# Kernel tuning notes

Hardware: AMD Instinct MI355X
Metric: run time of the kernel (lower is better)

## Reference

```python
import jax, jax.numpy as jnp
import numpy as np

E, D, H, B = 8, 64, 512, 32768  # n_experts, state_dim, hidden width, batch
IN = D + 3  # x, t, sin(omega*t), cos(omega*t)


def setup_inputs() -> dict:
    key = jax.random.key(0)
    ks = jax.random.split(key, 12)
    s = 0.02
    return {
        "t": jax.random.uniform(ks[0], (1,), dtype=jnp.float32),
        "x": jax.random.normal(ks[1], (B, D), dtype=jnp.float32),
        "expert_weights": jax.random.uniform(ks[2], (B, E), dtype=jnp.float32),
        "omega": jnp.arange(1, E + 1, dtype=jnp.float32),  # omega_i = i+1
        "W1": jax.random.normal(ks[3], (E, H, IN), dtype=jnp.float32) * s,
        "b1": jnp.zeros((E, H), dtype=jnp.float32),
        "W2": jax.random.normal(ks[4], (E, H, H), dtype=jnp.float32) * s,
        "b2": jnp.zeros((E, H), dtype=jnp.float32),
        "W3": jax.random.normal(ks[5], (E, H, H), dtype=jnp.float32) * s,
        "b3": jnp.zeros((E, H), dtype=jnp.float32),
        "W4": jax.random.normal(ks[6], (E, D, H), dtype=jnp.float32) * s,
        "b4": jnp.zeros((E, D), dtype=jnp.float32),
    }


def reference(t, x, expert_weights, omega, W1, b1, W2, b2, W3, b3, W4, b4):
    # Dense path of ExpertODEEnsemble.forward: all experts active.
    nB = x.shape[0]
    tb = jnp.broadcast_to(t, (nB,))                       # (B,)
    wt = omega[:, None] * tb[None, :]                     # (E, B)
    # Per-expert inputs: [x, t, sin(wt), cos(wt)] -> (E, B, D+3)
    xe = jnp.broadcast_to(x[None], (E, nB, D))
    te = jnp.broadcast_to(tb[None, :, None], (E, nB, 1))
    inp = jnp.concatenate([xe, te, jnp.sin(wt)[..., None], jnp.cos(wt)[..., None]], axis=-1)
    h = jnp.tanh(jnp.einsum('ebi,ehi->ebh', inp, W1) + b1[:, None, :])
    h = jnp.tanh(jnp.einsum('ebh,egh->ebg', h, W2) + b2[:, None, :])
    h = jnp.tanh(jnp.einsum('ebh,egh->ebg', h, W3) + b3[:, None, :])
    dyn = jnp.einsum('ebh,edh->ebd', h, W4) + b4[:, None, :]   # (E, B, D)
    # Weighted combine: sum_e w[b,e] * dyn[e,b,:]
    dx_dt = jnp.einsum('be,ebd->bd', expert_weights, dyn)
    return dx_dt
```

## Files before the change

### kernel.cpp

```cpp
#include <hip/hip_runtime.h>
#include <hip/hip_bf16.h>


typedef unsigned short ushort_t;
typedef unsigned int u32;
typedef unsigned long long u64;
typedef __attribute__((ext_vector_type(8))) short short8;
typedef __attribute__((ext_vector_type(4))) float floatx4;
typedef __attribute__((ext_vector_type(16))) float floatx16;
typedef __attribute__((ext_vector_type(4))) int intx4;

#define W1A_OFF 0u
#define W2A_OFF 524288u
#define W3A_OFF 4718592u
#define W4A_OFF 8912896u
#define XB_OFF  9437184u
#define B1E_OFF 13631488u

static __device__ __forceinline__ u32 pk2bf(float a, float b) {
  union { __hip_bfloat162 h; u32 u; } v;
  v.h = __float22bfloat162_rn(make_float2(a, b));
  return v.u;
}

static __device__ __forceinline__ float pade_tanh(float x) {
  float x2 = x * x;
  float num = __builtin_fmaf(x2, __builtin_fmaf(x2, 1.0f, 105.0f), 945.0f);
  float den = __builtin_fmaf(x2, __builtin_fmaf(x2, 15.0f, 420.0f), 945.0f);
  return x * num * __builtin_amdgcn_rcpf(den);
}

static __device__ __forceinline__ void ald16(const void* g, void* l) {
  __builtin_amdgcn_global_load_lds((__attribute__((address_space(1))) void*)g,
                                   (__attribute__((address_space(3))) void*)l,
                                   16, 0, 0);
}

static __device__ __forceinline__ floatx16 mfma32(short8 a, short8 b, floatx16 c) {
  return __builtin_amdgcn_mfma_f32_32x32x16_bf16(a, b, c, 0, 0, 0);
}

__global__ __launch_bounds__(256) void prep_kernel(
    const float* __restrict__ t, const float* __restrict__ x,
    const float* __restrict__ omega, const float* __restrict__ W1,
    const float* __restrict__ b1, const float* __restrict__ W2,
    const float* __restrict__ W3, const float* __restrict__ W4,
    char* __restrict__ ws) {
  int i = blockIdx.x * 256 + threadIdx.x;
  if (i < 32768) {
    int e = i >> 12, rem = i & 4095, outr = rem >> 3, kg = rem & 7;
    int lane = (outr & 31) | ((kg & 1) << 5);
    int w = outr >> 7, ol = (outr >> 5) & 3, kc = kg >> 1;
    int dest = e * 4096 + ((w * 4 + kc) * 4 + ol) * 64 + lane;
    const float* s = W1 + (e * 512 + outr) * 67 + kg * 8;
    ((intx4*)(ws + W1A_OFF))[dest] = (intx4){
        (int)pk2bf(s[0], s[1]), (int)pk2bf(s[2], s[3]),
        (int)pk2bf(s[4], s[5]), (int)pk2bf(s[6], s[7])};
    return;
  }
  i -= 32768;
  if (i < 262144) {
    int e = i >> 15, rem = i & 32767, outr = rem >> 6, kg = rem & 63;
    int lane = (outr & 31) | ((kg & 1) << 5);
    int w = outr >> 7, ol = (outr >> 5) & 3, kc = kg >> 1;
    int dest = e * 32768 + ((w * 32 + kc) * 4 + ol) * 64 + lane;
    const floatx4* s = (const floatx4*)(W2 + ((e << 9) + outr) * 512 + (kg << 3));
    floatx4 lo = s[0], hi = s[1];
    ((intx4*)(ws + W2A_OFF))[dest] = (intx4){
        (int)pk2bf(lo[0], lo[1]), (int)pk2bf(lo[2], lo[3]),
        (int)pk2bf(hi[0], hi[1]), (int)pk2bf(hi[2], hi[3])};
    return;
  }
  i -= 262144;
  if (i < 262144) {
    int e = i >> 15, rem = i & 32767, outr = rem >> 6, kg = rem & 63;
    int lane = (outr & 31) | ((kg & 1) << 5);
    int w = outr >> 7, ol = (outr >> 5) & 3, kc = kg >> 1;
    int dest = e * 32768 + ((w * 32 + kc) * 4 + ol) * 64 + lane;
    const floatx4* s = (const floatx4*)(W3 + ((e << 9) + outr) * 512 + (kg << 3));
    floatx4 lo = s[0], hi = s[1];
    ((intx4*)(ws + W3A_OFF))[dest] = (intx4){
        (int)pk2bf(lo[0], lo[1]), (int)pk2bf(lo[2], lo[3]),
        (int)pk2bf(hi[0], hi[1]), (int)pk2bf(hi[2], hi[3])};
    return;
  }
  i -= 262144;
  if (i < 32768) {
    int e = i >> 12, rem = i & 4095, outr = rem >> 6, kg = rem & 63;
    int lane = (outr & 31) | ((kg & 1) << 5);
    int o4 = outr >> 5, kc = kg >> 1;
    int dest = e * 4096 + (o4 * 32 + kc) * 64 + lane;
    const floatx4* s = (const floatx4*)(W4 + ((e << 6) + outr) * 512 + (kg << 3));
    floatx4 lo = s[0], hi = s[1];
    ((intx4*)(ws + W4A_OFF))[dest] = (intx4){
        (int)pk2bf(lo[0], lo[1]), (int)pk2bf(lo[2], lo[3]),
        (int)pk2bf(hi[0], hi[1]), (int)pk2bf(hi[2], hi[3])};
    return;
  }
  i -= 32768;
  if (i < 262144) {
    const floatx4* s = (const floatx4*)(x + i * 8);
    floatx4 lo = s[0], hi = s[1];
    ((intx4*)(ws + XB_OFF))[i] = (intx4){
        (int)pk2bf(lo[0], lo[1]), (int)pk2bf(lo[2], lo[3]),
        (int)pk2bf(hi[0], hi[1]), (int)pk2bf(hi[2], hi[3])};
    return;
  }
  i -= 262144;
  if (i < 4096) {
    float tv = t[0];
    int e = i >> 9;
    float om = omega[e];
    ((float*)(ws + B1E_OFF))[i] = b1[i] + tv * W1[i * 67 + 64]
        + sinf(om * tv) * W1[i * 67 + 65] + cosf(om * tv) * W1[i * 67 + 66];
  }
}


template <int NKC, bool WRAP>
static __device__ __forceinline__ void mlp_layer(
    const char* __restrict__ bsrc, char* __restrict__ dst,
    int lane, int w, int q1, int r31,
    const char* __restrict__ Abase, const float* __restrict__ bias) {
  const int voff = lane * 16;
  const char* sp = Abase + w * (NKC * 4096) + voff;
  const char* bp = bsrc + voff;

  floatx16 acc[4][2];
#pragma unroll
  for (int ol = 0; ol < 4; ++ol) {
    int fe0 = (4 * w + ol) * 32 + 4 * q1;
#pragma unroll
    for (int g = 0; g < 4; ++g) {
      floatx4 bv = *(const floatx4*)(bias + fe0 + 8 * g);
#pragma unroll
      for (int nt = 0; nt < 2; ++nt) {
        acc[ol][nt][4 * g + 0] = bv[0];
        acc[ol][nt][4 * g + 1] = bv[1];
        acc[ol][nt][4 * g + 2] = bv[2];
        acc[ol][nt][4 * g + 3] = bv[3];
      }
    }
  }
  short8 a0 = *(const short8*)(sp);
  short8 a1 = *(const short8*)(sp + 1024);
  short8 a2 = *(const short8*)(sp + 2048);
  short8 a3 = *(const short8*)(sp + 3072);
  sp += 4096;
  short8 b0 = *(const short8*)(bp);
  short8 b1 = *(const short8*)(bp + 1024);

#pragma unroll 4
  for (int kc = 0; kc < NKC; ++kc) {
    short8 an0 = *(const short8*)(sp);
    short8 an1 = *(const short8*)(sp + 1024);
    short8 an2 = *(const short8*)(sp + 2048);
    short8 an3 = *(const short8*)(sp + 3072);
    const char* bnext = WRAP ? (bsrc + voff + (((kc + 1) & (NKC - 1)) * 2112))
                             : (bp + 2112);
    short8 bn0 = *(const short8*)(bnext);
    short8 bn1 = *(const short8*)(bnext + 1024);
    acc[0][0] = mfma32(a0, b0, acc[0][0]);
    acc[1][0] = mfma32(a1, b0, acc[1][0]);
    acc[2][0] = mfma32(a2, b0, acc[2][0]);
    acc[3][0] = mfma32(a3, b0, acc[3][0]);
    acc[0][1] = mfma32(a0, b1, acc[0][1]);
    acc[1][1] = mfma32(a1, b1, acc[1][1]);
    acc[2][1] = mfma32(a2, b1, acc[2][1]);
    acc[3][1] = mfma32(a3, b1, acc[3][1]);
    a0 = an0; a1 = an1; a2 = an2; a3 = an3;
    b0 = bn0; b1 = bn1;
    sp += 4096;
    bp = bnext;
  }
  __syncthreads();
#pragma unroll
  for (int ol = 0; ol < 4; ++ol) {
    int o_abs = 4 * w + ol;
#pragma unroll
    for (int g = 0; g < 4; ++g) {
      int koct = o_abs * 4 + g;
      char* base = dst + ((((koct >> 1) * 132 + (koct & 1) * 32 + r31) << 4) + q1 * 8);
#pragma unroll
      for (int nt = 0; nt < 2; ++nt) {
        float v0 = pade_tanh(acc[ol][nt][4 * g + 0]);
        float v1 = pade_tanh(acc[ol][nt][4 * g + 1]);
        float v2 = pade_tanh(acc[ol][nt][4 * g + 2]);
        float v3 = pade_tanh(acc[ol][nt][4 * g + 3]);
        u32 lo = pk2bf(v0, v1), hi = pk2bf(v2, v3);
        *(u64*)(base + nt * 1024) = ((u64)hi << 32) | lo;
      }
    }
  }
  __syncthreads();
}

__global__ __launch_bounds__(256, 2) void fused_kernel(
    const char* __restrict__ ws, const float* __restrict__ b2,
    const float* __restrict__ b3, const float* __restrict__ b4,
    const float* __restrict__ ew, float* __restrict__ out) {
  __shared__ char smem[76032];
  char* xreg = smem + 67584;
  const int t = threadIdx.x, lane = t & 63, w = t >> 6;
  const int q1 = lane >> 5, r31 = lane & 31;
  const int xcd = blockIdx.x & 7;
  const int row0 = blockIdx.x << 6;
  const int voff = lane * 16;

  const ushort_t* xb = (const ushort_t*)(ws + XB_OFF);
  ald16(xb + (row0 + r31) * 64 + w * 16 + q1 * 8, xreg + (w * 132) * 16);
  ald16(xb + (row0 + 32 + r31) * 64 + w * 16 + q1 * 8, xreg + (w * 132 + 64) * 16);

  const int o4 = w & 1, nt4 = w >> 1;
  const int row_l4 = row0 + nt4 * 32 + r31;
  const int fe0 = o4 * 32 + 4 * q1;
  floatx16 out_acc = {};

  __syncthreads();

  for (int ei = 0; ei < 8; ++ei) {
    const int e = (xcd + ei) & 7;
    const float sc = ew[row_l4 * 8 + e];

    mlp_layer<4, true>(xreg, smem, lane, w, q1, r31,
                       ws + W1A_OFF + e * 65536,
                       (const float*)(ws + B1E_OFF) + e * 512);
    mlp_layer<32, false>(smem, smem, lane, w, q1, r31,
                         ws + W2A_OFF + e * 524288, b2 + e * 512);
    mlp_layer<32, false>(smem, smem, lane, w, q1, r31,
                         ws + W3A_OFF + e * 524288, b3 + e * 512);

    {
      const char* sp = ws + W4A_OFF + e * 65536 + o4 * 32768 + voff;
      const char* bp = smem + nt4 * 1024 + voff;
      floatx16 acc = {};
      short8 a = *(const short8*)(sp);
      short8 b = *(const short8*)(bp);
      sp += 1024;
#pragma unroll 4
      for (int kc = 0; kc < 32; ++kc) {
        short8 an = *(const short8*)(sp);
        short8 bn = *(const short8*)(bp + 2112);
        acc = mfma32(a, b, acc);
        a = an; b = bn;
        sp += 1024;
        bp += 2112;
      }
      const float* bpb = b4 + e * 64 + fe0;
#pragma unroll
      for (int g = 0; g < 4; ++g) {
        floatx4 bv = *(const floatx4*)(bpb + 8 * g);
        out_acc[4 * g + 0] += sc * (acc[4 * g + 0] + bv[0]);
        out_acc[4 * g + 1] += sc * (acc[4 * g + 1] + bv[1]);
        out_acc[4 * g + 2] += sc * (acc[4 * g + 2] + bv[2]);
        out_acc[4 * g + 3] += sc * (acc[4 * g + 3] + bv[3]);
      }
    }
  }

  float* orow = out + row_l4 * 64 + fe0;
#pragma unroll
  for (int g = 0; g < 4; ++g) {
    floatx4 v = {out_acc[4 * g + 0], out_acc[4 * g + 1],
                 out_acc[4 * g + 2], out_acc[4 * g + 3]};
    *(floatx4*)(orow + 8 * g) = v;
  }
}

extern "C" void kernel_launch(void* const* d_in, const int* in_sizes, int n_in,
                              void* d_out, int out_size, void* d_ws, size_t ws_size,
                              hipStream_t stream) {
  const float* t  = (const float*)d_in[0];
  const float* x  = (const float*)d_in[1];
  const float* ew = (const float*)d_in[2];
  const float* om = (const float*)d_in[3];
  const float* W1 = (const float*)d_in[4];
  const float* b1 = (const float*)d_in[5];
  const float* W2 = (const float*)d_in[6];
  const float* b2 = (const float*)d_in[7];
  const float* W3 = (const float*)d_in[8];
  const float* b3 = (const float*)d_in[9];
  const float* W4 = (const float*)d_in[10];
  const float* b4 = (const float*)d_in[11];
  char* ws = (char*)d_ws;
  float* out = (float*)d_out;
  (void)in_sizes; (void)n_in; (void)ws_size; (void)out_size;

  prep_kernel<<<3344, 256, 0, stream>>>(t, x, om, W1, b1, W2, W3, W4, ws);
  fused_kernel<<<512, 256, 0, stream>>>(ws, b2, b3, b4, ew, out);
}
```

Baseline: 450.1 us.

## Vectorize tanh with packed float2, linearize prep writes, change expert start order

```diff
diff --git a/kernel.cpp b/kernel.cpp
--- a/kernel.cpp
+++ b/kernel.cpp
@@ -6,6 +6,7 @@
 typedef unsigned int u32;
 typedef unsigned long long u64;
 typedef __attribute__((ext_vector_type(8))) short short8;
+typedef __attribute__((ext_vector_type(2))) float floatx2;
 typedef __attribute__((ext_vector_type(4))) float floatx4;
 typedef __attribute__((ext_vector_type(16))) float floatx16;
 typedef __attribute__((ext_vector_type(4))) int intx4;
@@ -23,11 +24,14 @@
   return v.u;
 }
 
-static __device__ __forceinline__ float pade_tanh(float x) {
-  float x2 = x * x;
-  float num = __builtin_fmaf(x2, __builtin_fmaf(x2, 1.0f, 105.0f), 945.0f);
-  float den = __builtin_fmaf(x2, __builtin_fmaf(x2, 15.0f, 420.0f), 945.0f);
-  return x * num * __builtin_amdgcn_rcpf(den);
+static __device__ __forceinline__ floatx2 pade_tanh2(floatx2 x) {
+  floatx2 x2 = x * x;
+  floatx2 num = x2 * (x2 + 105.0f) + 945.0f;
+  floatx2 den = x2 * (x2 * 15.0f + 420.0f) + 945.0f;
+  floatx2 r;
+  r[0] = __builtin_amdgcn_rcpf(den[0]);
+  r[1] = __builtin_amdgcn_rcpf(den[1]);
+  return x * num * r;
 }
 
 static __device__ __forceinline__ void ald16(const void* g, void* l) {
@@ -48,51 +52,55 @@
     char* __restrict__ ws) {
   int i = blockIdx.x * 256 + threadIdx.x;
   if (i < 32768) {
-    int e = i >> 12, rem = i & 4095, outr = rem >> 3, kg = rem & 7;
-    int lane = (outr & 31) | ((kg & 1) << 5);
-    int w = outr >> 7, ol = (outr >> 5) & 3, kc = kg >> 1;
-    int dest = e * 4096 + ((w * 4 + kc) * 4 + ol) * 64 + lane;
+    int e = i >> 12, d = i & 4095;
+    int lane = d & 63, q = d >> 6;
+    int ol = q & 3, kc = (q >> 2) & 3, w = q >> 4;
+    int outr = w * 128 + ol * 32 + (lane & 31);
+    int kg = kc * 2 + (lane >> 5);
     const float* s = W1 + (e * 512 + outr) * 67 + kg * 8;
-    ((intx4*)(ws + W1A_OFF))[dest] = (intx4){
+    ((intx4*)(ws + W1A_OFF))[i] = (intx4){
         (int)pk2bf(s[0], s[1]), (int)pk2bf(s[2], s[3]),
         (int)pk2bf(s[4], s[5]), (int)pk2bf(s[6], s[7])};
     return;
   }
   i -= 32768;
   if (i < 262144) {
-    int e = i >> 15, rem = i & 32767, outr = rem >> 6, kg = rem & 63;
-    int lane = (outr & 31) | ((kg & 1) << 5);
-    int w = outr >> 7, ol = (outr >> 5) & 3, kc = kg >> 1;
-    int dest = e * 32768 + ((w * 32 + kc) * 4 + ol) * 64 + lane;
+    int e = i >> 15, d = i & 32767;
+    int lane = d & 63, q = d >> 6;
+    int ol = q & 3, kc = (q >> 2) & 31, w = q >> 7;
+    int outr = w * 128 + ol * 32 + (lane & 31);
+    int kg = kc * 2 + (lane >> 5);
     const floatx4* s = (const floatx4*)(W2 + ((e << 9) + outr) * 512 + (kg << 3));
     floatx4 lo = s[0], hi = s[1];
-    ((intx4*)(ws + W2A_OFF))[dest] = (intx4){
+    ((intx4*)(ws + W2A_OFF))[i] = (intx4){
         (int)pk2bf(lo[0], lo[1]), (int)pk2bf(lo[2], lo[3]),
         (int)pk2bf(hi[0], hi[1]), (int)pk2bf(hi[2], hi[3])};
     return;
   }
   i -= 262144;
   if (i < 262144) {
-    int e = i >> 15, rem = i & 32767, outr = rem >> 6, kg = rem & 63;
-    int lane = (outr & 31) | ((kg & 1) << 5);
-    int w = outr >> 7, ol = (outr >> 5) & 3, kc = kg >> 1;
-    int dest = e * 32768 + ((w * 32 + kc) * 4 + ol) * 64 + lane;
+    int e = i >> 15, d = i & 32767;
+    int lane = d & 63, q = d >> 6;
+    int ol = q & 3, kc = (q >> 2) & 31, w = q >> 7;
+    int outr = w * 128 + ol * 32 + (lane & 31);
+    int kg = kc * 2 + (lane >> 5);
     const floatx4* s = (const floatx4*)(W3 + ((e << 9) + outr) * 512 + (kg << 3));
     floatx4 lo = s[0], hi = s[1];
-    ((intx4*)(ws + W3A_OFF))[dest] = (intx4){
+    ((intx4*)(ws + W3A_OFF))[i] = (intx4){
         (int)pk2bf(lo[0], lo[1]), (int)pk2bf(lo[2], lo[3]),
         (int)pk2bf(hi[0], hi[1]), (int)pk2bf(hi[2], hi[3])};
     return;
   }
   i -= 262144;
   if (i < 32768) {
-    int e = i >> 12, rem = i & 4095, outr = rem >> 6, kg = rem & 63;
-    int lane = (outr & 31) | ((kg & 1) << 5);
-    int o4 = outr >> 5, kc = kg >> 1;
-    int dest = e * 4096 + (o4 * 32 + kc) * 64 + lane;
+    int e = i >> 12, d = i & 4095;
+    int lane = d & 63, q = d >> 6;
+    int kc = q & 31, o4 = q >> 5;
+    int outr = o4 * 32 + (lane & 31);
+    int kg = kc * 2 + (lane >> 5);
     const floatx4* s = (const floatx4*)(W4 + ((e << 6) + outr) * 512 + (kg << 3));
     floatx4 lo = s[0], hi = s[1];
-    ((intx4*)(ws + W4A_OFF))[dest] = (intx4){
+    ((intx4*)(ws + W4A_OFF))[i] = (intx4){
         (int)pk2bf(lo[0], lo[1]), (int)pk2bf(lo[2], lo[3]),
         (int)pk2bf(hi[0], hi[1]), (int)pk2bf(hi[2], hi[3])};
     return;
@@ -156,10 +164,10 @@
     short8 an1 = *(const short8*)(sp + 1024);
     short8 an2 = *(const short8*)(sp + 2048);
     short8 an3 = *(const short8*)(sp + 3072);
-    const char* bnext = WRAP ? (bsrc + voff + (((kc + 1) & (NKC - 1)) * 2112))
-                             : (bp + 2112);
-    short8 bn0 = *(const short8*)(bnext);
-    short8 bn1 = *(const short8*)(bnext + 1024);
+    const char* bn = WRAP ? (bsrc + voff + (((kc + 1) & (NKC - 1)) * 2112))
+                          : (bp + 2112);
+    short8 bn0 = *(const short8*)(bn);
+    short8 bn1 = *(const short8*)(bn + 1024);
     acc[0][0] = mfma32(a0, b0, acc[0][0]);
     acc[1][0] = mfma32(a1, b0, acc[1][0]);
     acc[2][0] = mfma32(a2, b0, acc[2][0]);
@@ -171,7 +179,7 @@
     a0 = an0; a1 = an1; a2 = an2; a3 = an3;
     b0 = bn0; b1 = bn1;
     sp += 4096;
-    bp = bnext;
+    bp = bn;
   }
   __syncthreads();
 #pragma unroll
@@ -183,11 +191,11 @@
       char* base = dst + ((((koct >> 1) * 132 + (koct & 1) * 32 + r31) << 4) + q1 * 8);
 #pragma unroll
       for (int nt = 0; nt < 2; ++nt) {
-        float v0 = pade_tanh(acc[ol][nt][4 * g + 0]);
-        float v1 = pade_tanh(acc[ol][nt][4 * g + 1]);
-        float v2 = pade_tanh(acc[ol][nt][4 * g + 2]);
-        float v3 = pade_tanh(acc[ol][nt][4 * g + 3]);
-        u32 lo = pk2bf(v0, v1), hi = pk2bf(v2, v3);
+        floatx2 p0 = {acc[ol][nt][4 * g + 0], acc[ol][nt][4 * g + 1]};
+        floatx2 p1 = {acc[ol][nt][4 * g + 2], acc[ol][nt][4 * g + 3]};
+        floatx2 t0 = pade_tanh2(p0);
+        floatx2 t1 = pade_tanh2(p1);
+        u32 lo = pk2bf(t0[0], t0[1]), hi = pk2bf(t1[0], t1[1]);
         *(u64*)(base + nt * 1024) = ((u64)hi << 32) | lo;
       }
     }
@@ -203,7 +211,6 @@
   char* xreg = smem + 67584;
   const int t = threadIdx.x, lane = t & 63, w = t >> 6;
   const int q1 = lane >> 5, r31 = lane & 31;
-  const int xcd = blockIdx.x & 7;
   const int row0 = blockIdx.x << 6;
   const int voff = lane * 16;
 
@@ -218,8 +225,9 @@
 
   __syncthreads();
 
+  const int est = (blockIdx.x & 1) * 4;
   for (int ei = 0; ei < 8; ++ei) {
-    const int e = (xcd + ei) & 7;
+    const int e = (est + ei) & 7;
     const float sc = ew[row_l4 * 8 + e];
 
     mlp_layer<4, true>(xreg, smem, lane, w, q1, r31,
```

Measured after the change: 446.7 us. Within noise of the previous version (-0.7%).

## Use 128-row 8-wave blocks with LDS counter-based fine-grained inter-wave sync

Applied to the files above, without the earlier changes.

```diff
diff --git a/kernel.cpp b/kernel.cpp
--- a/kernel.cpp
+++ b/kernel.cpp
@@ -17,6 +17,10 @@
 #define XB_OFF  9437184u
 #define B1E_OFF 13631488u
 
+#define X_OFF_L 135168
+#define SYNC_OFF 152064
+#define SMEM_SZ 152128
+
 static __device__ __forceinline__ u32 pk2bf(float a, float b) {
   union { __hip_bfloat162 h; u32 u; } v;
   v.h = __float22bfloat162_rn(make_float2(a, b));
@@ -38,6 +42,16 @@
 
 static __device__ __forceinline__ floatx16 mfma32(short8 a, short8 b, floatx16 c) {
   return __builtin_amdgcn_mfma_f32_32x32x16_bf16(a, b, c, 0, 0, 0);
+}
+
+static __device__ __forceinline__ void waitge(const int* p, int tgt) {
+  while (*(volatile const int*)p < tgt) __builtin_amdgcn_s_sleep(1);
+  __asm__ __volatile__("" ::: "memory");
+}
+
+static __device__ __forceinline__ void bump(int* p, int lane) {
+  __asm__ __volatile__("s_waitcnt lgkmcnt(0)" ::: "memory");
+  if (lane == 0) atomicAdd(p, 1);
 }
 
 __global__ __launch_bounds__(256) void prep_kernel(
@@ -50,8 +64,8 @@
   if (i < 32768) {
     int e = i >> 12, rem = i & 4095, outr = rem >> 3, kg = rem & 7;
     int lane = (outr & 31) | ((kg & 1) << 5);
-    int w = outr >> 7, ol = (outr >> 5) & 3, kc = kg >> 1;
-    int dest = e * 4096 + ((w * 4 + kc) * 4 + ol) * 64 + lane;
+    int w = outr >> 6, ol = (outr >> 5) & 1, kc = kg >> 1;
+    int dest = e * 4096 + ((w * 4 + kc) * 2 + ol) * 64 + lane;
     const float* s = W1 + (e * 512 + outr) * 67 + kg * 8;
     ((intx4*)(ws + W1A_OFF))[dest] = (intx4){
         (int)pk2bf(s[0], s[1]), (int)pk2bf(s[2], s[3]),
@@ -62,8 +76,8 @@
   if (i < 262144) {
     int e = i >> 15, rem = i & 32767, outr = rem >> 6, kg = rem & 63;
     int lane = (outr & 31) | ((kg & 1) << 5);
-    int w = outr >> 7, ol = (outr >> 5) & 3, kc = kg >> 1;
-    int dest = e * 32768 + ((w * 32 + kc) * 4 + ol) * 64 + lane;
+    int w = outr >> 6, ol = (outr >> 5) & 1, kc = kg >> 1;
+    int dest = e * 32768 + ((w * 32 + kc) * 2 + ol) * 64 + lane;
     const floatx4* s = (const floatx4*)(W2 + ((e << 9) + outr) * 512 + (kg << 3));
     floatx4 lo = s[0], hi = s[1];
     ((intx4*)(ws + W2A_OFF))[dest] = (intx4){
@@ -75,8 +89,8 @@
   if (i < 262144) {
     int e = i >> 15, rem = i & 32767, outr = rem >> 6, kg = rem & 63;
     int lane = (outr & 31) | ((kg & 1) << 5);
-    int w = outr >> 7, ol = (outr >> 5) & 3, kc = kg >> 1;
-    int dest = e * 32768 + ((w * 32 + kc) * 4 + ol) * 64 + lane;
+    int w = outr >> 6, ol = (outr >> 5) & 1, kc = kg >> 1;
+    int dest = e * 32768 + ((w * 32 + kc) * 2 + ol) * 64 + lane;
     const floatx4* s = (const floatx4*)(W3 + ((e << 9) + outr) * 512 + (kg << 3));
     floatx4 lo = s[0], hi = s[1];
     ((intx4*)(ws + W3A_OFF))[dest] = (intx4){
@@ -117,24 +131,24 @@
 }
 
 
-template <int NKC, bool WRAP>
+template <int NKC, bool ISX>
 static __device__ __forceinline__ void mlp_layer(
-    const char* __restrict__ bsrc, char* __restrict__ dst,
-    int lane, int w, int q1, int r31,
-    const char* __restrict__ Abase, const float* __restrict__ bias) {
+    const char* __restrict__ bsrc, char* __restrict__ act,
+    int* kcp, int* pub, int lane, int w, int q1, int r31,
+    const char* __restrict__ Abase, const float* __restrict__ bias,
+    int pub_tgt, int tgt_cov, int tgt_oth, int khm, bool do_epi_wait) {
   const int voff = lane * 16;
-  const char* sp = Abase + w * (NKC * 4096) + voff;
-  const char* bp = bsrc + voff;
-
-  floatx16 acc[4][2];
-#pragma unroll
-  for (int ol = 0; ol < 4; ++ol) {
-    int fe0 = (4 * w + ol) * 32 + 4 * q1;
+  const char* sp = Abase + w * (NKC * 2048) + voff;
+
+  floatx16 acc[2][4];
+#pragma unroll
+  for (int ol = 0; ol < 2; ++ol) {
+    int fe0 = w * 64 + ol * 32 + 4 * q1;
 #pragma unroll
     for (int g = 0; g < 4; ++g) {
       floatx4 bv = *(const floatx4*)(bias + fe0 + 8 * g);
 #pragma unroll
-      for (int nt = 0; nt < 2; ++nt) {
+      for (int nt = 0; nt < 4; ++nt) {
         acc[ol][nt][4 * g + 0] = bv[0];
         acc[ol][nt][4 * g + 1] = bv[1];
         acc[ol][nt][4 * g + 2] = bv[2];
@@ -144,45 +158,54 @@
   }
   short8 a0 = *(const short8*)(sp);
   short8 a1 = *(const short8*)(sp + 1024);
-  short8 a2 = *(const short8*)(sp + 2048);
-  short8 a3 = *(const short8*)(sp + 3072);
-  sp += 4096;
-  short8 b0 = *(const short8*)(bp);
-  short8 b1 = *(const short8*)(bp + 1024);
-
-#pragma unroll 4
-  for (int kc = 0; kc < NKC; ++kc) {
-    short8 an0 = *(const short8*)(sp);
-    short8 an1 = *(const short8*)(sp + 1024);
-    short8 an2 = *(const short8*)(sp + 2048);
-    short8 an3 = *(const short8*)(sp + 3072);
-    const char* bnext = WRAP ? (bsrc + voff + (((kc + 1) & (NKC - 1)) * 2112))
-                             : (bp + 2112);
-    short8 bn0 = *(const short8*)(bnext);
-    short8 bn1 = *(const short8*)(bnext + 1024);
-    acc[0][0] = mfma32(a0, b0, acc[0][0]);
-    acc[1][0] = mfma32(a1, b0, acc[1][0]);
-    acc[2][0] = mfma32(a2, b0, acc[2][0]);
-    acc[3][0] = mfma32(a3, b0, acc[3][0]);
-    acc[0][1] = mfma32(a0, b1, acc[0][1]);
-    acc[1][1] = mfma32(a1, b1, acc[1][1]);
-    acc[2][1] = mfma32(a2, b1, acc[2][1]);
-    acc[3][1] = mfma32(a3, b1, acc[3][1]);
-    a0 = an0; a1 = an1; a2 = an2; a3 = an3;
-    b0 = bn0; b1 = bn1;
-    sp += 4096;
-    bp = bnext;
-  }
-  __syncthreads();
-#pragma unroll
-  for (int ol = 0; ol < 4; ++ol) {
-    int o_abs = 4 * w + ol;
+  sp += 2048;
+
+  const int NG = NKC / 4;
+#pragma unroll 1
+  for (int g = 0; g < NG; ++g) {
+    if (!ISX) waitge(pub + g, pub_tgt);
+    const char* gb = bsrc + g * (4 * 4224) + voff;
+    short8 b0 = *(const short8*)(gb);
+    short8 b1v = *(const short8*)(gb + 1024);
+    short8 b2 = *(const short8*)(gb + 2048);
+    short8 b3 = *(const short8*)(gb + 3072);
+#pragma unroll
+    for (int j = 0; j < 4; ++j) {
+      short8 an0 = *(const short8*)(sp);
+      short8 an1 = *(const short8*)(sp + 1024);
+      sp += 2048;
+      const char* bn = gb + ((j + 1) & 3) * 4224;
+      short8 bn0 = *(const short8*)(bn);
+      short8 bn1 = *(const short8*)(bn + 1024);
+      short8 bn2 = *(const short8*)(bn + 2048);
+      short8 bn3 = *(const short8*)(bn + 3072);
+      acc[0][0] = mfma32(a0, b0, acc[0][0]);
+      acc[0][1] = mfma32(a0, b1v, acc[0][1]);
+      acc[0][2] = mfma32(a0, b2, acc[0][2]);
+      acc[0][3] = mfma32(a0, b3, acc[0][3]);
+      acc[1][0] = mfma32(a1, b0, acc[1][0]);
+      acc[1][1] = mfma32(a1, b1v, acc[1][1]);
+      acc[1][2] = mfma32(a1, b2, acc[1][2]);
+      acc[1][3] = mfma32(a1, b3, acc[1][3]);
+      a0 = an0; a1 = an1;
+      b0 = bn0; b1v = bn1; b2 = bn2; b3 = bn3;
+    }
+    bump(kcp + w, lane);
+  }
+
+  if (do_epi_wait) {
+    for (int w2 = 0; w2 < 8; ++w2)
+      waitge(kcp + w2, ((w2 >> 2) == khm) ? tgt_cov : tgt_oth);
+  }
+#pragma unroll
+  for (int ol = 0; ol < 2; ++ol) {
 #pragma unroll
     for (int g = 0; g < 4; ++g) {
-      int koct = o_abs * 4 + g;
-      char* base = dst + ((((koct >> 1) * 132 + (koct & 1) * 32 + r31) << 4) + q1 * 8);
-#pragma unroll
-      for (int nt = 0; nt < 2; ++nt) {
+      int ko = ol * 4 + g;
+      char* base = act + (4 * w + (ko >> 1)) * 4224
+                   + (((ko & 1) * 32 + r31) << 4) + q1 * 8;
+#pragma unroll
+      for (int nt = 0; nt < 4; ++nt) {
         float v0 = pade_tanh(acc[ol][nt][4 * g + 0]);
         float v1 = pade_tanh(acc[ol][nt][4 * g + 1]);
         float v2 = pade_tanh(acc[ol][nt][4 * g + 2]);
@@ -192,78 +215,122 @@
       }
     }
   }
-  __syncthreads();
-}
-
-__global__ __launch_bounds__(256, 2) void fused_kernel(
+  bump(pub + w, lane);
+}
+
+extern "C" __global__ __launch_bounds__(512) void fused_kernel(
     const char* __restrict__ ws, const float* __restrict__ b2,
     const float* __restrict__ b3, const float* __restrict__ b4,
     const float* __restrict__ ew, float* __restrict__ out) {
-  __shared__ char smem[76032];
-  char* xreg = smem + 67584;
+  extern __shared__ char smem[];
+  char* act = smem;
+  char* xreg = smem + X_OFF_L;
+  int* kcp = (int*)(smem + SYNC_OFF);
+  int* pub = kcp + 8;
+
   const int t = threadIdx.x, lane = t & 63, w = t >> 6;
   const int q1 = lane >> 5, r31 = lane & 31;
-  const int xcd = blockIdx.x & 7;
-  const int row0 = blockIdx.x << 6;
+  const int row0 = blockIdx.x << 7;
   const int voff = lane * 16;
 
+  if (t < 16) ((int*)(smem + SYNC_OFF))[t] = 0;
+
   const ushort_t* xb = (const ushort_t*)(ws + XB_OFF);
-  ald16(xb + (row0 + r31) * 64 + w * 16 + q1 * 8, xreg + (w * 132) * 16);
-  ald16(xb + (row0 + 32 + r31) * 64 + w * 16 + q1 * 8, xreg + (w * 132 + 64) * 16);
-
-  const int o4 = w & 1, nt4 = w >> 1;
-  const int row_l4 = row0 + nt4 * 32 + r31;
-  const int fe0 = o4 * 32 + 4 * q1;
-  floatx16 out_acc = {};
-
+#pragma unroll
+  for (int s = 0; s < 2; ++s) {
+    int u = w + 8 * s, v = u >> 2, nt = u & 3;
+    ald16(xb + (row0 + nt * 32 + r31) * 64 + (2 * v + q1) * 8,
+          xreg + v * 4224 + nt * 1024);
+  }
   __syncthreads();
 
-  for (int ei = 0; ei < 8; ++ei) {
-    const int e = (xcd + ei) & 7;
-    const float sc = ew[row_l4 * 8 + e];
-
-    mlp_layer<4, true>(xreg, smem, lane, w, q1, r31,
+  const int rt = w & 3, kh = w >> 2;
+  const int row_l4 = row0 + rt * 32 + r31;
+  floatx16 oacc[2] = {};
+
+  for (int e = 0; e < 8; ++e) {
+    mlp_layer<4, true>(xreg, act, kcp, pub, lane, w, q1, r31,
                        ws + W1A_OFF + e * 65536,
-                       (const float*)(ws + B1E_OFF) + e * 512);
-    mlp_layer<32, false>(smem, smem, lane, w, q1, r31,
-                         ws + W2A_OFF + e * 524288, b2 + e * 512);
-    mlp_layer<32, false>(smem, smem, lane, w, q1, r31,
-                         ws + W3A_OFF + e * 524288, b3 + e * 512);
+                       (const float*)(ws + B1E_OFF) + e * 512,
+                       0, 21 * e + (w & 3) - 3, 21 * e + w - 11, w >> 2, e > 0);
+    mlp_layer<32, false>(act, act, kcp, pub, lane, w, q1, r31,
+                         ws + W2A_OFF + e * 524288, b2 + e * 512,
+                         3 * e + 1, 21 * e + w + 2, 21 * e + w + 2, 0, true);
+    mlp_layer<32, false>(act, act, kcp, pub, lane, w, q1, r31,
+                         ws + W3A_OFF + e * 524288, b3 + e * 512,
+                         3 * e + 2, 21 * e + w + 10, 21 * e + w + 10, 0, true);
 
     {
-      const char* sp = ws + W4A_OFF + e * 65536 + o4 * 32768 + voff;
-      const char* bp = smem + nt4 * 1024 + voff;
-      floatx16 acc = {};
-      short8 a = *(const short8*)(sp);
-      short8 b = *(const short8*)(bp);
-      sp += 1024;
-#pragma unroll 4
-      for (int kc = 0; kc < 32; ++kc) {
-        short8 an = *(const short8*)(sp);
-        short8 bn = *(const short8*)(bp + 2112);
-        acc = mfma32(a, b, acc);
-        a = an; b = bn;
-        sp += 1024;
-        bp += 2112;
-      }
-      const float* bpb = b4 + e * 64 + fe0;
+      const char* spA = ws + W4A_OFF + e * 65536 + voff;
+      const float sc = ew[row_l4 * 8 + e];
+      floatx16 acc4[2] = {};
+      int kc0 = kh * 16;
+      short8 a0 = *(const short8*)(spA + kc0 * 1024);
+      short8 a1 = *(const short8*)(spA + 32768 + kc0 * 1024);
+#pragma unroll 1
+      for (int gl = 0; gl < 4; ++gl) {
+        int g = kh * 4 + gl;
+        waitge(pub + g, 3 * e + 3);
+        const char* gb = act + g * (4 * 4224) + rt * 1024 + voff;
+        short8 b = *(const short8*)(gb);
+#pragma unroll
+        for (int j = 0; j < 4; ++j) {
+          int kc = g * 4 + j;
+          short8 an0 = *(const short8*)(spA + (kc + 1) * 1024);
+          short8 an1 = *(const short8*)(spA + 32768 + (kc + 1) * 1024);
+          short8 bn = *(const short8*)(gb + ((j + 1) & 3) * 4224);
+          acc4[0] = mfma32(a0, b, acc4[0]);
+          acc4[1] = mfma32(a1, b, acc4[1]);
+          a0 = an0; a1 = an1; b = bn;
+        }
+        bump(kcp + w, lane);
+      }
+      if (kh == 0) {
+        const float* bp = b4 + e * 64;
+#pragma unroll
+        for (int ol = 0; ol < 2; ++ol) {
+          int fe0 = ol * 32 + 4 * q1;
+#pragma unroll
+          for (int g = 0; g < 4; ++g) {
+            floatx4 bv = *(const floatx4*)(bp + fe0 + 8 * g);
+            oacc[ol][4 * g + 0] += sc * (acc4[ol][4 * g + 0] + bv[0]);
+            oacc[ol][4 * g + 1] += sc * (acc4[ol][4 * g + 1] + bv[1]);
+            oacc[ol][4 * g + 2] += sc * (acc4[ol][4 * g + 2] + bv[2]);
+            oacc[ol][4 * g + 3] += sc * (acc4[ol][4 * g + 3] + bv[3]);
+          }
+        }
+      } else {
+#pragma unroll
+        for (int ol = 0; ol < 2; ++ol)
+#pragma unroll
+          for (int i = 0; i < 16; ++i) oacc[ol][i] += sc * acc4[ol][i];
+      }
+    }
+  }
+
+  __syncthreads();
+  if (kh == 1) {
+#pragma unroll
+    for (int ol = 0; ol < 2; ++ol)
 #pragma unroll
       for (int g = 0; g < 4; ++g) {
-        floatx4 bv = *(const floatx4*)(bpb + 8 * g);
-        out_acc[4 * g + 0] += sc * (acc[4 * g + 0] + bv[0]);
-        out_acc[4 * g + 1] += sc * (acc[4 * g + 1] + bv[1]);
-        out_acc[4 * g + 2] += sc * (acc[4 * g + 2] + bv[2]);
-        out_acc[4 * g + 3] += sc * (acc[4 * g + 3] + bv[3]);
-      }
-    }
-  }
-
-  float* orow = out + row_l4 * 64 + fe0;
-#pragma unroll
-  for (int g = 0; g < 4; ++g) {
-    floatx4 v = {out_acc[4 * g + 0], out_acc[4 * g + 1],
-                 out_acc[4 * g + 2], out_acc[4 * g + 3]};
-    *(floatx4*)(orow + 8 * g) = v;
+        floatx4 p = {oacc[ol][4 * g + 0], oacc[ol][4 * g + 1],
+                     oacc[ol][4 * g + 2], oacc[ol][4 * g + 3]};
+        *(floatx4*)(act + rt * 8192 + ol * 4096 + g * 1024 + lane * 16) = p;
+      }
+  }
+  __syncthreads();
+  if (kh == 0) {
+    float* orow = out + row_l4 * 64;
+#pragma unroll
+    for (int ol = 0; ol < 2; ++ol)
+#pragma unroll
+      for (int g = 0; g < 4; ++g) {
+        floatx4 p = *(const floatx4*)(act + rt * 8192 + ol * 4096 + g * 1024 + lane * 16);
+        floatx4 v = {oacc[ol][4 * g + 0] + p[0], oacc[ol][4 * g + 1] + p[1],
+                     oacc[ol][4 * g + 2] + p[2], oacc[ol][4 * g + 3] + p[3]};
+        *(floatx4*)(orow + ol * 32 + 8 * g + 4 * q1) = v;
+      }
   }
 }
 
@@ -286,6 +353,12 @@
   float* out = (float*)d_out;
   (void)in_sizes; (void)n_in; (void)ws_size; (void)out_size;
 
+  static int smem_set = 0;
+  if (!smem_set) {
+    hipFuncSetAttribute((const void*)fused_kernel,
+                        hipFuncAttributeMaxDynamicSharedMemorySize, SMEM_SZ);
+    smem_set = 1;
+  }
   prep_kernel<<<3344, 256, 0, stream>>>(t, x, om, W1, b1, W2, W3, W4, ws);
-  fused_kernel<<<512, 256, 0, stream>>>(ws, b2, b3, b4, ew, out);
-}
+  fused_kernel<<<256, 512, SMEM_SZ, stream>>>(ws, b2, b3, b4, ew, out);
+}
```

Result: faster. 441.3 us (-2.0%).
